# Kernel optimization log

Hardware: AMD Instinct MI355X
Metric: run time of the kernel (lower is better)

Reference implementation:

```python
import jax, jax.numpy as jnp
import numpy as np
import math

B, S, H, D = 8, 2048, 1024, 64  # batch, seq_len, hidden_dim, head_size

def setup_inputs() -> dict:
    key = jax.random.key(0)
    ks = jax.random.split(key, 7)
    lim = 1.0 / math.sqrt(H)  # torch Linear default init bound
    return {
        "x":  jax.random.normal(ks[0], (B, S, H), dtype=jnp.float32),
        "Wq": jax.random.uniform(ks[1], (H, D), jnp.float32, -lim, lim),
        "bq": jax.random.uniform(ks[2], (D,),   jnp.float32, -lim, lim),
        "Wk": jax.random.uniform(ks[3], (H, D), jnp.float32, -lim, lim),
        "bk": jax.random.uniform(ks[4], (D,),   jnp.float32, -lim, lim),
        "Wv": jax.random.uniform(ks[5], (H, D), jnp.float32, -lim, lim),
        "bv": jax.random.uniform(ks[6], (D,),   jnp.float32, -lim, lim),
    }

def reference(x, Wq, bq, Wk, bk, Wv, bv):
    # x: [B, S, H]
    q = x @ Wq + bq          # [B, S, D]
    k = x @ Wk + bk          # [B, S, D]
    v = x @ Wv + bv          # [B, S, D]
    scores = jnp.einsum("bsd,btd->bst", q, k)       # [B, S, S]
    causal = jnp.tril(jnp.ones((S, S), dtype=bool))
    scores = jnp.where(causal, scores, -jnp.inf)
    # NOTE: original module (faithfully) applies softmax FIRST, then divides
    # by sqrt(hidden_dim) -- it does NOT scale logits before softmax.
    weight = jax.nn.softmax(scores, axis=-1) / jnp.sqrt(jnp.float32(x.shape[-1]))
    # dropout p=0.0 -> identity
    return jnp.einsum("bst,btd->bsd", weight, v)     # [B, S, D]
```

## Files before the change

kernel.cpp:

```cpp
#include <hip/hip_runtime.h>


typedef float     f32x4 __attribute__((ext_vector_type(4)));
typedef _Float16  f16x8 __attribute__((ext_vector_type(8)));
typedef _Float16  f16x4 __attribute__((ext_vector_type(4)));

#define L2E 1.44269504088896340736f

__global__ __launch_bounds__(256) void wt_prep(const float* __restrict__ Wq,
                                               const float* __restrict__ Wk,
                                               const float* __restrict__ Wv,
                                               _Float16* __restrict__ WtF) {
  const int w  = blockIdx.x >> 4;
  const int kt = blockIdx.x & 15;
  const float* src = (w == 0) ? Wq : (w == 1 ? Wk : Wv);
  __shared__ _Float16 ls[64][72];
  const int t = threadIdx.x;
  {
    int rr = t >> 4;
    int c4 = (t & 15) * 4;
    #pragma unroll
    for (int ri = 0; ri < 4; ++ri) {
      int k = rr + ri * 16;
      f32x4 f = *(const f32x4*)&src[(size_t)(kt * 64 + k) * 64 + c4];
      #pragma unroll
      for (int j = 0; j < 4; ++j) ls[k][c4 + j] = (_Float16)f[j];
    }
  }
  __syncthreads();
  const int lane = t & 63, l16 = lane & 15, quad = lane >> 4;
  #pragma unroll
  for (int h = 0; h < 2; ++h) {
    int fid     = h * 4 + (t >> 6);
    int kstep_l = fid >> 2;
    int ntl     = fid & 3;
    int nt      = w * 4 + ntl;
    int kstep   = kt * 2 + kstep_l;
    f16x8 o;
    #pragma unroll
    for (int j = 0; j < 8; ++j) o[j] = ls[kstep_l * 32 + quad * 8 + j][ntl * 16 + l16];
    *(f16x8*)&WtF[((size_t)(kstep * 12 + nt) * 64 + lane) * 8] = o;
  }
}

__global__ __launch_bounds__(768) void qkv_gemm(const float* __restrict__ x,
                                                const _Float16* __restrict__ WtF,
                                                const float* __restrict__ bq,
                                                const float* __restrict__ bk,
                                                const float* __restrict__ bv,
                                                _Float16* __restrict__ qo,
                                                _Float16* __restrict__ ko,
                                                _Float16* __restrict__ vt) {
  __shared__ _Float16 xs[32 * 1024];
  const int tid  = threadIdx.x;
  const int wave = tid >> 6, lane = tid & 63;
  const int l16  = lane & 15, quad = lane >> 4;
  const int mhalf = wave / 6;
  const int ngrp  = wave - mhalf * 6;
  const int m0    = blockIdx.x * 32;

  if (tid < 512) {
    int row   = tid >> 4;
    int cbase = (tid & 15) * 4;
    const float* xrow = x + (size_t)(m0 + row) * 1024;
    int key = row & 7;
    #pragma unroll
    for (int j = 0; j < 16; ++j) {
      int col = cbase + j * 64;
      f32x4 f = *(const f32x4*)&xrow[col];
      f16x4 hh;
      #pragma unroll
      for (int e = 0; e < 4; ++e) hh[e] = (_Float16)f[e];
      int g   = col >> 3;
      int sub = col & 7;
      *(f16x4*)&xs[(size_t)row * 1024 + (size_t)((g ^ key) << 3) + sub] = hh;
    }
  }
  __syncthreads();

  f32x4 acc0 = (f32x4){0.f,0.f,0.f,0.f};
  f32x4 acc1 = (f32x4){0.f,0.f,0.f,0.f};
  const int arow = mhalf * 16 + l16;
  const _Float16* abase = xs + (size_t)arow * 1024;
  const int akey = arow & 7;
  const _Float16* wbase = WtF + ((size_t)(ngrp * 2) * 64 + lane) * 8;

  #pragma unroll 4
  for (int kstep = 0; kstep < 32; ++kstep) {
    f16x8 a = *(const f16x8*)(abase + (((kstep * 4 + quad) ^ akey) << 3));
    const _Float16* wk = wbase + (size_t)kstep * (12 * 64 * 8);
    f16x8 b0 = *(const f16x8*)(wk);
    f16x8 b1 = *(const f16x8*)(wk + 512);
    acc0 = __builtin_amdgcn_mfma_f32_16x16x32_f16(a, b0, acc0, 0, 0, 0);
    acc1 = __builtin_amdgcn_mfma_f32_16x16x32_f16(a, b1, acc1, 0, 0, 0);
  }

  f32x4 accs[2] = {acc0, acc1};
  #pragma unroll
  for (int i = 0; i < 2; ++i) {
    int nt  = ngrp * 2 + i;
    int col = nt * 16 + l16;
    float bias = (nt < 4) ? bq[col] : (nt < 8) ? bk[col - 64] : bv[col - 128];
    #pragma unroll
    for (int r = 0; r < 4; ++r) {
      int m = m0 + mhalf * 16 + quad * 4 + r;
      _Float16 hv = (_Float16)(accs[i][r] + bias);
      if (nt < 4)      qo[(size_t)m * 64 + col] = hv;
      else if (nt < 8) ko[(size_t)m * 64 + (col - 64)] = hv;
      else {
        int b = m >> 11, s = m & 2047;
        vt[((size_t)b * 64 + (col - 128)) * 2048 + s] = hv;
      }
    }
  }
}

__global__ __launch_bounds__(256) void attn(const _Float16* __restrict__ q,
                                            const _Float16* __restrict__ k,
                                            const _Float16* __restrict__ vt,
                                            _Float16* __restrict__ po,
                                            float* __restrict__ pm,
                                            float* __restrict__ pl) {
  const int bid = 575 - blockIdx.x;
  const int b   = blockIdx.y;
  int g = 0;
  #pragma unroll
  for (int gg = 0; gg < 7; ++gg) if (bid >= 8 * (gg + 1) * (gg + 2)) g = gg + 1;
  const int r   = bid - 8 * g * (g + 1);
  const int qi  = r / (g + 1);
  const int qt  = 16 * g + qi;
  const int s   = r - qi * (g + 1);
  const int q0  = qt * 16, kvend = q0 + 16;

  const int tid  = threadIdx.x;
  const int wave = tid >> 6, lane = tid & 63;
  const int l16  = lane & 15, quad = lane >> 4;
  const int kv0  = s * 256 + wave * 64;

  __shared__ float ow[4][64][17];
  __shared__ float mw[4][16], lw[4][16];
  _Float16* Plw = (_Float16*)&ow[wave][0][0];

  float m = -1e30f, l = 0.f;
  f32x4 o[4];
  #pragma unroll
  for (int i = 0; i < 4; ++i) o[i] = (f32x4){0.f, 0.f, 0.f, 0.f};

  if (kv0 < kvend) {
    const _Float16* qb = q  + (size_t)b * 2048 * 64;
    const _Float16* kb = k  + (size_t)b * 2048 * 64;
    const _Float16* vb = vt + (size_t)b * 64 * 2048;
    f16x8 qf0 = *(const f16x8*)&qb[(q0 + l16) * 64 + quad * 8];
    f16x8 qf1 = *(const f16x8*)&qb[(q0 + l16) * 64 + 32 + quad * 8];

    f32x4 sc[4];
    #pragma unroll
    for (int t = 0; t < 4; ++t) {
      int kvc = kv0 + t * 16;
      if (kvc < kvend) {
        f16x8 kf0 = *(const f16x8*)&kb[(kvc + l16) * 64 + quad * 8];
        f16x8 kf1 = *(const f16x8*)&kb[(kvc + l16) * 64 + 32 + quad * 8];
        f32x4 c = (f32x4){0.f, 0.f, 0.f, 0.f};
        c = __builtin_amdgcn_mfma_f32_16x16x32_f16(kf0, qf0, c, 0, 0, 0);
        c = __builtin_amdgcn_mfma_f32_16x16x32_f16(kf1, qf1, c, 0, 0, 0);
        sc[t] = c;
      } else sc[t] = (f32x4){-1e30f, -1e30f, -1e30f, -1e30f};
    }
    if (kv0 + 63 > q0) {
      #pragma unroll
      for (int t = 0; t < 4; ++t) {
        #pragma unroll
        for (int rr = 0; rr < 4; ++rr) {
          int skv = kv0 + t * 16 + quad * 4 + rr;
          if (skv > q0 + l16) sc[t][rr] = -1e30f;
        }
      }
    }
    float mx = sc[0][0];
    #pragma unroll
    for (int t = 0; t < 4; ++t)
      #pragma unroll
      for (int rr = 0; rr < 4; ++rr) mx = fmaxf(mx, sc[t][rr]);
    mx = fmaxf(mx, __shfl_xor(mx, 16, 64));
    mx = fmaxf(mx, __shfl_xor(mx, 32, 64));
    m = mx;
    float sum = 0.f;
    #pragma unroll
    for (int t = 0; t < 4; ++t)
      #pragma unroll
      for (int rr = 0; rr < 4; ++rr) {
        float e = exp2f((sc[t][rr] - m) * L2E);
        sc[t][rr] = e;
        sum += e;
      }
    sum += __shfl_xor(sum, 16, 64);
    sum += __shfl_xor(sum, 32, 64);
    l = sum;
    #pragma unroll
    for (int t = 0; t < 4; ++t)
      #pragma unroll
      for (int rr = 0; rr < 4; ++rr)
        Plw[l16 * 72 + t * 16 + quad * 4 + rr] = (_Float16)sc[t][rr];
    asm volatile("s_waitcnt lgkmcnt(0)" ::: "memory");
    f16x8 p0 = *(const f16x8*)&Plw[l16 * 72 + quad * 8];
    f16x8 p1 = *(const f16x8*)&Plw[l16 * 72 + 32 + quad * 8];
    #pragma unroll
    for (int dt = 0; dt < 4; ++dt) {
      f16x8 v0 = *(const f16x8*)&vb[(size_t)(dt * 16 + l16) * 2048 + kv0 + quad * 8];
      f16x8 v1 = *(const f16x8*)&vb[(size_t)(dt * 16 + l16) * 2048 + kv0 + 32 + quad * 8];
      o[dt] = __builtin_amdgcn_mfma_f32_16x16x32_f16(v0, p0, o[dt], 0, 0, 0);
      o[dt] = __builtin_amdgcn_mfma_f32_16x16x32_f16(v1, p1, o[dt], 0, 0, 0);
    }
  }

  __syncthreads();
  #pragma unroll
  for (int dt = 0; dt < 4; ++dt)
    #pragma unroll
    for (int rr = 0; rr < 4; ++rr)
      ow[wave][dt * 16 + quad * 4 + rr][l16] = o[dt][rr];
  if (quad == 0) { mw[wave][l16] = m; lw[wave][l16] = l; }
  __syncthreads();

  {
    int qrow = tid >> 4, d4 = (tid & 15) * 4;
    float m0v = mw[0][qrow], m1v = mw[1][qrow], m2v = mw[2][qrow], m3v = mw[3][qrow];
    float M = fmaxf(fmaxf(m0v, m1v), fmaxf(m2v, m3v));
    float w0 = exp2f((m0v - M) * L2E), w1 = exp2f((m1v - M) * L2E);
    float w2 = exp2f((m2v - M) * L2E), w3 = exp2f((m3v - M) * L2E);
    float L = w0 * lw[0][qrow] + w1 * lw[1][qrow] + w2 * lw[2][qrow] + w3 * lw[3][qrow];
    size_t pid = (size_t)b * 576 + bid;
    f16x4 oh;
    #pragma unroll
    for (int j = 0; j < 4; ++j)
      oh[j] = (_Float16)(w0 * ow[0][d4 + j][qrow] + w1 * ow[1][d4 + j][qrow]
                       + w2 * ow[2][d4 + j][qrow] + w3 * ow[3][d4 + j][qrow]);
    *(f16x4*)&po[pid * 1024 + (size_t)qrow * 64 + d4] = oh;
    if ((tid & 15) == 0) { pm[pid * 16 + qrow] = M; pl[pid * 16 + qrow] = L; }
  }
}

__global__ __launch_bounds__(256) void attn_merge(const _Float16* __restrict__ po,
                                                  const float* __restrict__ pm,
                                                  const float* __restrict__ pl,
                                                  float* __restrict__ out) {
  const int qt = blockIdx.x, b = blockIdx.y;
  const int g = qt >> 4, S = g + 1;
  const size_t base = (size_t)b * 576 + (size_t)(g + 1) * (8 * g + (qt & 15));
  const int t = threadIdx.x, qrow = t >> 4, d4 = (t & 15) * 4;

  float M = -1e30f;
  for (int s = 0; s < S; ++s) M = fmaxf(M, pm[(base + s) * 16 + qrow]);
  float L = 0.f;
  float O0 = 0.f, O1 = 0.f, O2 = 0.f, O3 = 0.f;
  for (int s = 0; s < S; ++s) {
    float w = exp2f((pm[(base + s) * 16 + qrow] - M) * L2E);
    L += w * pl[(base + s) * 16 + qrow];
    f16x4 ov = *(const f16x4*)&po[(base + s) * 1024 + (size_t)qrow * 64 + d4];
    O0 += w * (float)ov[0]; O1 += w * (float)ov[1];
    O2 += w * (float)ov[2]; O3 += w * (float)ov[3];
  }
  float inv = 1.0f / (L * 32.0f);
  f32x4 res = (f32x4){O0 * inv, O1 * inv, O2 * inv, O3 * inv};
  *(f32x4*)&out[((size_t)b * 2048 + qt * 16 + qrow) * 64 + d4] = res;
}

extern "C" void kernel_launch(void* const* d_in, const int* in_sizes, int n_in,
                              void* d_out, int out_size, void* d_ws, size_t ws_size,
                              hipStream_t stream) {
  const float* x  = (const float*)d_in[0];
  const float* Wq = (const float*)d_in[1];
  const float* bq = (const float*)d_in[2];
  const float* Wk = (const float*)d_in[3];
  const float* bk = (const float*)d_in[4];
  const float* Wv = (const float*)d_in[5];
  const float* bv = (const float*)d_in[6];
  float* out = (float*)d_out;

  _Float16* WtF = (_Float16*)d_ws;
  _Float16* qo  = WtF + 192 * 1024;
  _Float16* ko  = qo + 16384 * 64;
  _Float16* vt  = ko + 16384 * 64;
  _Float16* po  = vt + 8 * 64 * 2048;
  float*    pm  = (float*)(po + (size_t)4608 * 1024);
  float*    pl  = pm + 4608 * 16;

  hipLaunchKernelGGL(wt_prep,    dim3(48),       dim3(256), 0, stream, Wq, Wk, Wv, WtF);
  hipLaunchKernelGGL(qkv_gemm,   dim3(512),      dim3(768), 0, stream, x, WtF, bq, bk, bv, qo, ko, vt);
  hipLaunchKernelGGL(attn,       dim3(576, 8),   dim3(256), 0, stream, qo, ko, vt, po, pm, pl);
  hipLaunchKernelGGL(attn_merge, dim3(128, 8),   dim3(256), 0, stream, po, pm, pl, out);
}
```

Measured before the change: 162.9 us.

## Stream x directly in QKV GEMM, write single-split attention output directly

The QKV GEMM no longer stages x into shared memory. Each 256-thread block handles 16 rows, loads fp32 x straight from global memory, converts it to fp16 in registers, and computes 3 N-tiles per wave. This drops the LDS staging and barrier and allows higher occupancy, but each of the four waves in a block now reads the same x rows. The attention grid is flattened with batch interleaved, the P tile is stored to LDS with vectorized writes, and query tiles with only one KV split write the final output themselves. The merge kernel therefore skips those tiles.

```diff
diff --git a/kernel.cpp b/kernel.cpp
--- a/kernel.cpp
+++ b/kernel.cpp
@@ -43,67 +43,52 @@
   }
 }
 
-__global__ __launch_bounds__(768) void qkv_gemm(const float* __restrict__ x,
-                                                const _Float16* __restrict__ WtF,
-                                                const float* __restrict__ bq,
-                                                const float* __restrict__ bk,
-                                                const float* __restrict__ bv,
-                                                _Float16* __restrict__ qo,
-                                                _Float16* __restrict__ ko,
-                                                _Float16* __restrict__ vt) {
-  __shared__ _Float16 xs[32 * 1024];
+__global__ __launch_bounds__(256, 4) void qkv_gemm(const float* __restrict__ x,
+                                                   const _Float16* __restrict__ WtF,
+                                                   const float* __restrict__ bq,
+                                                   const float* __restrict__ bk,
+                                                   const float* __restrict__ bv,
+                                                   _Float16* __restrict__ qo,
+                                                   _Float16* __restrict__ ko,
+                                                   _Float16* __restrict__ vt) {
   const int tid  = threadIdx.x;
   const int wave = tid >> 6, lane = tid & 63;
   const int l16  = lane & 15, quad = lane >> 4;
-  const int mhalf = wave / 6;
-  const int ngrp  = wave - mhalf * 6;
-  const int m0    = blockIdx.x * 32;
-
-  if (tid < 512) {
-    int row   = tid >> 4;
-    int cbase = (tid & 15) * 4;
-    const float* xrow = x + (size_t)(m0 + row) * 1024;
-    int key = row & 7;
-    #pragma unroll
-    for (int j = 0; j < 16; ++j) {
-      int col = cbase + j * 64;
-      f32x4 f = *(const f32x4*)&xrow[col];
-      f16x4 hh;
-      #pragma unroll
-      for (int e = 0; e < 4; ++e) hh[e] = (_Float16)f[e];
-      int g   = col >> 3;
-      int sub = col & 7;
-      *(f16x4*)&xs[(size_t)row * 1024 + (size_t)((g ^ key) << 3) + sub] = hh;
-    }
-  }
-  __syncthreads();
+  const int ngrp = wave;
+  const int m0   = blockIdx.x * 16;
 
   f32x4 acc0 = (f32x4){0.f,0.f,0.f,0.f};
   f32x4 acc1 = (f32x4){0.f,0.f,0.f,0.f};
-  const int arow = mhalf * 16 + l16;
-  const _Float16* abase = xs + (size_t)arow * 1024;
-  const int akey = arow & 7;
-  const _Float16* wbase = WtF + ((size_t)(ngrp * 2) * 64 + lane) * 8;
+  f32x4 acc2 = (f32x4){0.f,0.f,0.f,0.f};
+
+  const float* ap = x + (size_t)(m0 + l16) * 1024 + quad * 8;
+  const _Float16* wbase = WtF + ((size_t)(ngrp * 3) * 64 + lane) * 8;
 
   #pragma unroll 4
   for (int kstep = 0; kstep < 32; ++kstep) {
-    f16x8 a = *(const f16x8*)(abase + (((kstep * 4 + quad) ^ akey) << 3));
+    f32x4 a0 = *(const f32x4*)(ap + kstep * 32);
+    f32x4 a1 = *(const f32x4*)(ap + kstep * 32 + 4);
     const _Float16* wk = wbase + (size_t)kstep * (12 * 64 * 8);
     f16x8 b0 = *(const f16x8*)(wk);
     f16x8 b1 = *(const f16x8*)(wk + 512);
+    f16x8 b2 = *(const f16x8*)(wk + 1024);
+    f16x8 a;
+    #pragma unroll
+    for (int j = 0; j < 4; ++j) { a[j] = (_Float16)a0[j]; a[4 + j] = (_Float16)a1[j]; }
     acc0 = __builtin_amdgcn_mfma_f32_16x16x32_f16(a, b0, acc0, 0, 0, 0);
     acc1 = __builtin_amdgcn_mfma_f32_16x16x32_f16(a, b1, acc1, 0, 0, 0);
-  }
-
-  f32x4 accs[2] = {acc0, acc1};
-  #pragma unroll
-  for (int i = 0; i < 2; ++i) {
-    int nt  = ngrp * 2 + i;
+    acc2 = __builtin_amdgcn_mfma_f32_16x16x32_f16(a, b2, acc2, 0, 0, 0);
+  }
+
+  f32x4 accs[3] = {acc0, acc1, acc2};
+  #pragma unroll
+  for (int i = 0; i < 3; ++i) {
+    int nt  = ngrp * 3 + i;
     int col = nt * 16 + l16;
     float bias = (nt < 4) ? bq[col] : (nt < 8) ? bk[col - 64] : bv[col - 128];
     #pragma unroll
     for (int r = 0; r < 4; ++r) {
-      int m = m0 + mhalf * 16 + quad * 4 + r;
+      int m = m0 + quad * 4 + r;
       _Float16 hv = (_Float16)(accs[i][r] + bias);
       if (nt < 4)      qo[(size_t)m * 64 + col] = hv;
       else if (nt < 8) ko[(size_t)m * 64 + (col - 64)] = hv;
@@ -120,9 +105,11 @@
                                             const _Float16* __restrict__ vt,
                                             _Float16* __restrict__ po,
                                             float* __restrict__ pm,
-                                            float* __restrict__ pl) {
-  const int bid = 575 - blockIdx.x;
-  const int b   = blockIdx.y;
+                                            float* __restrict__ pl,
+                                            float* __restrict__ out) {
+  const int blk = blockIdx.x;
+  const int b   = blk & 7;
+  const int bid = 575 - (blk >> 3);
   int g = 0;
   #pragma unroll
   for (int gg = 0; gg < 7; ++gg) if (bid >= 8 * (gg + 1) * (gg + 2)) g = gg + 1;
@@ -150,16 +137,16 @@
     const _Float16* qb = q  + (size_t)b * 2048 * 64;
     const _Float16* kb = k  + (size_t)b * 2048 * 64;
     const _Float16* vb = vt + (size_t)b * 64 * 2048;
-    f16x8 qf0 = *(const f16x8*)&qb[(q0 + l16) * 64 + quad * 8];
-    f16x8 qf1 = *(const f16x8*)&qb[(q0 + l16) * 64 + 32 + quad * 8];
+    f16x8 qf0 = *(const f16x8*)&qb[(size_t)(q0 + l16) * 64 + quad * 8];
+    f16x8 qf1 = *(const f16x8*)&qb[(size_t)(q0 + l16) * 64 + 32 + quad * 8];
 
     f32x4 sc[4];
     #pragma unroll
     for (int t = 0; t < 4; ++t) {
       int kvc = kv0 + t * 16;
       if (kvc < kvend) {
-        f16x8 kf0 = *(const f16x8*)&kb[(kvc + l16) * 64 + quad * 8];
-        f16x8 kf1 = *(const f16x8*)&kb[(kvc + l16) * 64 + 32 + quad * 8];
+        f16x8 kf0 = *(const f16x8*)&kb[(size_t)(kvc + l16) * 64 + quad * 8];
+        f16x8 kf1 = *(const f16x8*)&kb[(size_t)(kvc + l16) * 64 + 32 + quad * 8];
         f32x4 c = (f32x4){0.f, 0.f, 0.f, 0.f};
         c = __builtin_amdgcn_mfma_f32_16x16x32_f16(kf0, qf0, c, 0, 0, 0);
         c = __builtin_amdgcn_mfma_f32_16x16x32_f16(kf1, qf1, c, 0, 0, 0);
@@ -197,10 +184,12 @@
     sum += __shfl_xor(sum, 32, 64);
     l = sum;
     #pragma unroll
-    for (int t = 0; t < 4; ++t)
-      #pragma unroll
-      for (int rr = 0; rr < 4; ++rr)
-        Plw[l16 * 72 + t * 16 + quad * 4 + rr] = (_Float16)sc[t][rr];
+    for (int t = 0; t < 4; ++t) {
+      f16x4 ph;
+      #pragma unroll
+      for (int rr = 0; rr < 4; ++rr) ph[rr] = (_Float16)sc[t][rr];
+      *(f16x4*)&Plw[l16 * 72 + t * 16 + quad * 4] = ph;
+    }
     asm volatile("s_waitcnt lgkmcnt(0)" ::: "memory");
     f16x8 p0 = *(const f16x8*)&Plw[l16 * 72 + quad * 8];
     f16x8 p1 = *(const f16x8*)&Plw[l16 * 72 + 32 + quad * 8];
@@ -229,14 +218,26 @@
     float w0 = exp2f((m0v - M) * L2E), w1 = exp2f((m1v - M) * L2E);
     float w2 = exp2f((m2v - M) * L2E), w3 = exp2f((m3v - M) * L2E);
     float L = w0 * lw[0][qrow] + w1 * lw[1][qrow] + w2 * lw[2][qrow] + w3 * lw[3][qrow];
-    size_t pid = (size_t)b * 576 + bid;
-    f16x4 oh;
-    #pragma unroll
-    for (int j = 0; j < 4; ++j)
-      oh[j] = (_Float16)(w0 * ow[0][d4 + j][qrow] + w1 * ow[1][d4 + j][qrow]
-                       + w2 * ow[2][d4 + j][qrow] + w3 * ow[3][d4 + j][qrow]);
-    *(f16x4*)&po[pid * 1024 + (size_t)qrow * 64 + d4] = oh;
-    if ((tid & 15) == 0) { pm[pid * 16 + qrow] = M; pl[pid * 16 + qrow] = L; }
+    float O0 = w0 * ow[0][d4 + 0][qrow] + w1 * ow[1][d4 + 0][qrow]
+             + w2 * ow[2][d4 + 0][qrow] + w3 * ow[3][d4 + 0][qrow];
+    float O1 = w0 * ow[0][d4 + 1][qrow] + w1 * ow[1][d4 + 1][qrow]
+             + w2 * ow[2][d4 + 1][qrow] + w3 * ow[3][d4 + 1][qrow];
+    float O2 = w0 * ow[0][d4 + 2][qrow] + w1 * ow[1][d4 + 2][qrow]
+             + w2 * ow[2][d4 + 2][qrow] + w3 * ow[3][d4 + 2][qrow];
+    float O3 = w0 * ow[0][d4 + 3][qrow] + w1 * ow[1][d4 + 3][qrow]
+             + w2 * ow[2][d4 + 3][qrow] + w3 * ow[3][d4 + 3][qrow];
+    if (g == 0) {
+      float inv = 1.0f / (L * 32.0f);
+      f32x4 res = (f32x4){O0 * inv, O1 * inv, O2 * inv, O3 * inv};
+      *(f32x4*)&out[((size_t)b * 2048 + q0 + qrow) * 64 + d4] = res;
+    } else {
+      size_t pid = (size_t)b * 576 + bid;
+      f16x4 oh;
+      oh[0] = (_Float16)O0; oh[1] = (_Float16)O1;
+      oh[2] = (_Float16)O2; oh[3] = (_Float16)O3;
+      *(f16x4*)&po[pid * 1024 + (size_t)qrow * 64 + d4] = oh;
+      if ((tid & 15) == 0) { pm[pid * 16 + qrow] = M; pl[pid * 16 + qrow] = L; }
+    }
   }
 }
 
@@ -244,7 +245,7 @@
                                                   const float* __restrict__ pm,
                                                   const float* __restrict__ pl,
                                                   float* __restrict__ out) {
-  const int qt = blockIdx.x, b = blockIdx.y;
+  const int qt = 16 + blockIdx.x, b = blockIdx.y;
   const int g = qt >> 4, S = g + 1;
   const size_t base = (size_t)b * 576 + (size_t)(g + 1) * (8 * g + (qt & 15));
   const int t = threadIdx.x, qrow = t >> 4, d4 = (t & 15) * 4;
@@ -285,8 +286,8 @@
   float*    pm  = (float*)(po + (size_t)4608 * 1024);
   float*    pl  = pm + 4608 * 16;
 
-  hipLaunchKernelGGL(wt_prep,    dim3(48),       dim3(256), 0, stream, Wq, Wk, Wv, WtF);
-  hipLaunchKernelGGL(qkv_gemm,   dim3(512),      dim3(768), 0, stream, x, WtF, bq, bk, bv, qo, ko, vt);
-  hipLaunchKernelGGL(attn,       dim3(576, 8),   dim3(256), 0, stream, qo, ko, vt, po, pm, pl);
-  hipLaunchKernelGGL(attn_merge, dim3(128, 8),   dim3(256), 0, stream, po, pm, pl, out);
-}
+  hipLaunchKernelGGL(wt_prep,    dim3(48),      dim3(256), 0, stream, Wq, Wk, Wv, WtF);
+  hipLaunchKernelGGL(qkv_gemm,   dim3(1024),    dim3(256), 0, stream, x, WtF, bq, bk, bv, qo, ko, vt);
+  hipLaunchKernelGGL(attn,       dim3(4608),    dim3(256), 0, stream, qo, ko, vt, po, pm, pl, out);
+  hipLaunchKernelGGL(attn_merge, dim3(112, 8),  dim3(256), 0, stream, po, pm, pl, out);
+}
```

After: 185.2 us. 13.8% more time.
